# Optimization experiments

Hardware: AMD Instinct MI355X
Metric: run time of the kernel (lower is better)

Reference implementation:

```python
import jax, jax.numpy as jnp
import numpy as np
import math

BATCH, L, H, P = 8, 2048, 1024, 512
DT_MIN, DT_MAX = 1e-3, 1e-1
STEP_RESCALE = 1.0


def setup_inputs() -> dict:
    key = jax.random.key(0)
    ks = jax.random.split(key, 8)
    signal = jax.random.normal(ks[0], (BATCH, L, H), dtype=jnp.float32)
    prev_state = jnp.zeros((BATCH, P), dtype=jnp.float32)
    # S5-style init: Lambda_re < 0, Lambda_im = pi * k
    Lambda_re = -0.5 * jnp.ones((P,), dtype=jnp.float32)
    Lambda_im = math.pi * jnp.arange(P, dtype=jnp.float32)
    # B stored as real (P,H,2) -> complex B_tilde; lecun scale 1/sqrt(H)
    B = jax.random.normal(ks[1], (P, H, 2), dtype=jnp.float32) / math.sqrt(H)
    # C stored as real (H,P,2) -> complex C_tilde; lecun scale 1/sqrt(P)
    C = jax.random.normal(ks[2], (H, P, 2), dtype=jnp.float32) / math.sqrt(P)
    D = jax.random.normal(ks[3], (H,), dtype=jnp.float32)
    u = jax.random.uniform(ks[4], (P, 1), dtype=jnp.float32)
    log_step = u * (math.log(DT_MAX) - math.log(DT_MIN)) + math.log(DT_MIN)
    return {"signal": signal, "prev_state": prev_state,
            "Lambda_re": Lambda_re, "Lambda_im": Lambda_im,
            "B": B, "C": C, "D": D, "log_step": log_step}


def _binop(qi, qj):
    # parallel-scan combine for diagonal linear recurrence x_t = A_t x_{t-1} + b_t
    A_i, b_i = qi
    A_j, b_j = qj
    return (A_j * A_i, b_j + A_j * b_i)


def reference(signal, prev_state, Lambda_re, Lambda_im, B, C, D, log_step):
    Lambda = Lambda_re + 1j * Lambda_im                      # (P,) complex
    B_tilde = B[..., 0] + 1j * B[..., 1]                     # (P,H)
    C_tilde = C[..., 0] + 1j * C[..., 1]                     # (H,P)
    step = STEP_RESCALE * jnp.exp(log_step[:, 0])            # (P,)
    # zero-order hold discretization
    Lambda_bar = jnp.exp(Lambda * step)                      # (P,)
    B_bar = ((Lambda_bar - 1.0) / Lambda)[:, None] * B_tilde # (P,H)
    # Bu elements: (BATCH, L, P) complex
    Bu = jnp.einsum('blh,ph->blp', signal.astype(B_bar.dtype), B_bar)
    # A elements: Lambda_bar tiled over time; first element carries prev_state
    A_first = (Lambda_bar[None, :] * prev_state.astype(Lambda_bar.dtype))[:, None, :]
    A_rest = jnp.broadcast_to(Lambda_bar, (signal.shape[0], signal.shape[1] - 1, Lambda_bar.shape[0]))
    A = jnp.concatenate([A_first, A_rest], axis=1)           # (BATCH, L, P)
    _, xs = jax.lax.associative_scan(_binop, (A, Bu), axis=1)  # xs: (BATCH, L, P)
    # conj_sym=True -> 2 * Re(C_tilde @ x), plus feedthrough D*u
    y = 2.0 * jnp.einsum('blp,hp->blh', xs, C_tilde).real + D * signal
    state = xs[:, -1]                                        # (BATCH, P) complex
    return y, state
```

## Files before the change

### kernel.cpp

```cpp
#include <hip/hip_runtime.h>
#include <math.h>

#define L_SEQ   2048
#define BATCH_N 8
#define H_DIM   1024
#define P_DIM   512
#define M_DIM   (BATCH_N * L_SEQ)
#define N2      1024
#define NC      16
#define T_CHUNK 128

typedef __attribute__((ext_vector_type(8))) __bf16 bf16x8;
typedef __attribute__((ext_vector_type(4))) float f32x4;

__device__ __forceinline__ unsigned f2bf_bits(float f) {
    unsigned u = __builtin_bit_cast(unsigned, f);
    return (u + 0x7fffu + ((u >> 16) & 1u)) >> 16;
}
__device__ __forceinline__ float bf_lo(unsigned v) {
    return __builtin_bit_cast(float, v << 16);
}
__device__ __forceinline__ float bf_hi(unsigned v) {
    return __builtin_bit_cast(float, v & 0xffff0000u);
}
__device__ __forceinline__ float bf2f(unsigned short u) {
    return __builtin_bit_cast(float, (unsigned)u << 16);
}

#define ASYNC_COPY16(gsrc, ldst)                                            \
    __builtin_amdgcn_global_load_lds(                                       \
        (__attribute__((address_space(1))) void*)(gsrc),                    \
        (__attribute__((address_space(3))) void*)(ldst), 16, 0, 0)

__global__ void setup_lam(const float* __restrict__ Lre_in,
                          const float* __restrict__ Lim_in,
                          const float* __restrict__ log_step,
                          float* __restrict__ lam) {
    int p = blockIdx.x * blockDim.x + threadIdx.x;
    if (p >= P_DIM) return;
    float step = expf(log_step[p]);
    float c = Lre_in[p];
    float d = Lim_in[p];
    float mag = expf(c * step);
    float ang = d * step;
    float lr = mag * cosf(ang);
    float li = mag * sinf(ang);
    float a = lr - 1.0f, b = li;
    float inv = 1.0f / (c * c + d * d);
    lam[p]             = lr;
    lam[P_DIM + p]     = li;
    lam[2 * P_DIM + p] = (a * c + b * d) * inv;
    lam[3 * P_DIM + p] = (b * c - a * d) * inv;
}

__global__ void build_W(const float* __restrict__ B,
                        const float* __restrict__ C,
                        const float* __restrict__ lam,
                        unsigned short* __restrict__ W1,
                        unsigned short* __restrict__ W2) {
    int idx = blockIdx.x * blockDim.x + threadIdx.x;
    if (idx < P_DIM * H_DIM) {
        int p = idx >> 10;
        int h = idx & (H_DIM - 1);
        float bre = B[(size_t)idx * 2];
        float bim = B[(size_t)idx * 2 + 1];
        float gre = lam[2 * P_DIM + p];
        float gim = lam[3 * P_DIM + p];
        W1[(size_t)p * H_DIM + h]           = (unsigned short)f2bf_bits(gre * bre - gim * bim);
        W1[(size_t)(P_DIM + p) * H_DIM + h] = (unsigned short)f2bf_bits(gre * bim + gim * bre);
    } else {
        int j = idx - P_DIM * H_DIM;
        int h = j >> 9;
        int p = j & (P_DIM - 1);
        float cre = C[(size_t)j * 2];
        float cim = C[(size_t)j * 2 + 1];
        W2[(size_t)h * N2 + p]         = (unsigned short)f2bf_bits( 2.0f * cre);
        W2[(size_t)h * N2 + P_DIM + p] = (unsigned short)f2bf_bits(-2.0f * cim);
    }
}

__global__ void convert_sig(const float* __restrict__ in,
                            unsigned short* __restrict__ out) {
    size_t i = ((size_t)blockIdx.x * 256 + threadIdx.x) * 4;
    float4 v = *(const float4*)(in + i);
    ushort4 o;
    o.x = (unsigned short)f2bf_bits(v.x);
    o.y = (unsigned short)f2bf_bits(v.y);
    o.z = (unsigned short)f2bf_bits(v.z);
    o.w = (unsigned short)f2bf_bits(v.w);
    *(ushort4*)(out + i) = o;
}

template <int MODE>
__global__ __launch_bounds__(256) void gemm_mfma(
    const unsigned short* __restrict__ A,
    const unsigned short* __restrict__ W,
    void* __restrict__ Out, int K,
    const float* __restrict__ Dvec, const unsigned short* __restrict__ SigBf)
{
    __shared__ unsigned short smem[128 * 32 * 2];
    unsigned short* As = smem;
    unsigned short* Ws = smem + 128 * 32;

    const int tid  = threadIdx.x;
    const int lane = tid & 63;
    const int wid  = tid >> 6;
    const int wm   = wid >> 1;
    const int wn   = wid & 1;

    const int id  = blockIdx.x;
    const int xcd = id & 7;
    const int j   = id >> 3;
    const int mb  = xcd * 16 + (j >> 3);
    const int nb  = j & 7;
    const int m0 = mb * 128;
    const int n0 = nb * 128;

    const int r0 = tid >> 2;
    const int kq = (tid & 3) * 8;
    const unsigned short* Ag0 = A + (size_t)(m0 + r0) * K + kq;
    const unsigned short* Ag1 = Ag0 + (size_t)64 * K;
    const unsigned short* Wg0 = W + (size_t)(n0 + r0) * K + kq;
    const unsigned short* Wg1 = Wg0 + (size_t)64 * K;
    unsigned short* Ad0 = As + (size_t)(wid * 64) * 8;
    unsigned short* Ad1 = As + (size_t)(256 + wid * 64) * 8;
    unsigned short* Wd0 = Ws + (size_t)(wid * 64) * 8;
    unsigned short* Wd1 = Ws + (size_t)(256 + wid * 64) * 8;

    const int fr = lane & 15;
    const int fq = lane >> 4;

    f32x4 acc[4][4] = {};

    for (int k0 = 0; k0 < K; k0 += 32) {
        __syncthreads();
        ASYNC_COPY16(Ag0 + k0, Ad0);
        ASYNC_COPY16(Ag1 + k0, Ad1);
        ASYNC_COPY16(Wg0 + k0, Wd0);
        ASYNC_COPY16(Wg1 + k0, Wd1);
        __syncthreads();

        bf16x8 af[4], wf[4];
        #pragma unroll
        for (int mi = 0; mi < 4; ++mi)
            af[mi] = *(const bf16x8*)&As[(size_t)(wm * 64 + mi * 16 + fr) * 32 + fq * 8];
        #pragma unroll
        for (int ni = 0; ni < 4; ++ni)
            wf[ni] = *(const bf16x8*)&Ws[(size_t)(wn * 64 + ni * 16 + fr) * 32 + fq * 8];
        #pragma unroll
        for (int mi = 0; mi < 4; ++mi)
            #pragma unroll
            for (int ni = 0; ni < 4; ++ni)
                acc[mi][ni] = __builtin_amdgcn_mfma_f32_16x16x32_bf16(
                    af[mi], wf[ni], acc[mi][ni], 0, 0, 0);
    }

    if (MODE == 0) {
        unsigned short* T = smem;
        #pragma unroll
        for (int h = 0; h < 2; ++h) {
            __syncthreads();
            if (wm == h) {
                #pragma unroll
                for (int mi = 0; mi < 4; ++mi)
                    #pragma unroll
                    for (int ni = 0; ni < 4; ++ni)
                        #pragma unroll
                        for (int r = 0; r < 4; ++r) {
                            int lrow = mi * 16 + fq * 4 + r;
                            int lcol = wn * 64 + ni * 16 + fr;
                            T[lrow * 128 + lcol] =
                                (unsigned short)f2bf_bits(acc[mi][ni][r]);
                        }
            }
            __syncthreads();
            #pragma unroll
            for (int jj = 0; jj < 4; ++jj) {
                int chunk = jj * 256 + tid;
                int row = chunk >> 4;
                int co  = (chunk & 15) * 8;
                *(ulonglong2*)((unsigned short*)Out +
                    (size_t)(m0 + h * 64 + row) * 1024 + n0 + co) =
                    *(const ulonglong2*)&T[row * 128 + co];
            }
        }
    } else {
        #pragma unroll
        for (int mi = 0; mi < 4; ++mi) {
            #pragma unroll
            for (int ni = 0; ni < 4; ++ni) {
                #pragma unroll
                for (int r = 0; r < 4; ++r) {
                    int row = m0 + wm * 64 + mi * 16 + fq * 4 + r;
                    int col = n0 + wn * 64 + ni * 16 + fr;
                    float v = acc[mi][ni][r];
                    v = fmaf(Dvec[col], bf2f(SigBf[(size_t)row * 1024 + col]), v);
                    ((float*)Out)[(size_t)row * 1024 + col] = v;
                }
            }
        }
    }
}

__global__ __launch_bounds__(256) void scan_sums(
    const unsigned short* __restrict__ Bu, const float* __restrict__ lam,
    float* __restrict__ S)
{
    int b = blockIdx.x, c = blockIdx.y, t = threadIdx.x;
    int p0 = 2 * t, p1 = 2 * t + 1;
    float lr0 = lam[p0], li0 = lam[P_DIM + p0];
    float lr1 = lam[p1], li1 = lam[P_DIM + p1];
    const unsigned* base =
        (const unsigned*)(Bu + ((size_t)b * L_SEQ + (size_t)c * T_CHUNK) * N2);
    float xr0 = 0, xi0 = 0, xr1 = 0, xi1 = 0;
    for (int j0 = 0; j0 < T_CHUNK; j0 += 8) {
        unsigned R[8], I[8];
        #pragma unroll
        for (int j = 0; j < 8; ++j) {
            R[j] = base[(size_t)(j0 + j) * 512 + t];
            I[j] = base[(size_t)(j0 + j) * 512 + 256 + t];
        }
        #pragma unroll
        for (int j = 0; j < 8; ++j) {
            float nr0 = fmaf(lr0, xr0, fmaf(-li0, xi0, bf_lo(R[j])));
            float ni0 = fmaf(lr0, xi0, fmaf( li0, xr0, bf_lo(I[j])));
            float nr1 = fmaf(lr1, xr1, fmaf(-li1, xi1, bf_hi(R[j])));
            float ni1 = fmaf(lr1, xi1, fmaf( li1, xr1, bf_hi(I[j])));
            xr0 = nr0; xi0 = ni0; xr1 = nr1; xi1 = ni1;
        }
    }
    float* Sb = S + ((size_t)(b * NC + c) * 2) * P_DIM;
    Sb[p0] = xr0; Sb[p1] = xr1;
    Sb[P_DIM + p0] = xi0; Sb[P_DIM + p1] = xi1;
}

__global__ __launch_bounds__(512) void scan_carry(
    const float* __restrict__ S, const float* __restrict__ lam,
    float* __restrict__ CIN)
{
    int b = blockIdx.x, p = threadIdx.x;
    float lr = lam[p], li = lam[P_DIM + p];
    float pr = lr, pi = li;
    #pragma unroll
    for (int i = 0; i < 7; ++i) {
        float nr = pr * pr - pi * pi;
        float ni = 2.0f * pr * pi;
        pr = nr; pi = ni;
    }
    float cr = 0, ci = 0;
    for (int c = 0; c < NC; ++c) {
        float* Cb = CIN + ((size_t)(b * NC + c) * 2) * P_DIM;
        Cb[p] = cr; Cb[P_DIM + p] = ci;
        const float* Sb = S + ((size_t)(b * NC + c) * 2) * P_DIM;
        float sr = Sb[p], si = Sb[P_DIM + p];
        float nr = fmaf(pr, cr, fmaf(-pi, ci, sr));
        float ni = fmaf(pr, ci, fmaf( pi, cr, si));
        cr = nr; ci = ni;
    }
}

__global__ __launch_bounds__(256) void scan_apply(
    unsigned short* __restrict__ Bu, const float* __restrict__ lam,
    const float* __restrict__ CIN, float* __restrict__ out_state,
    int interleaved)
{
    int b = blockIdx.x, c = blockIdx.y, t = threadIdx.x;
    int p0 = 2 * t, p1 = 2 * t + 1;
    float lr0 = lam[p0], li0 = lam[P_DIM + p0];
    float lr1 = lam[p1], li1 = lam[P_DIM + p1];
    const float* Cb = CIN + ((size_t)(b * NC + c) * 2) * P_DIM;
    float xr0 = Cb[p0], xi0 = Cb[P_DIM + p0];
    float xr1 = Cb[p1], xi1 = Cb[P_DIM + p1];
    unsigned* base =
        (unsigned*)(Bu + ((size_t)b * L_SEQ + (size_t)c * T_CHUNK) * N2);
    for (int j0 = 0; j0 < T_CHUNK; j0 += 8) {
        unsigned R[8], I[8];
        #pragma unroll
        for (int j = 0; j < 8; ++j) {
            R[j] = base[(size_t)(j0 + j) * 512 + t];
            I[j] = base[(size_t)(j0 + j) * 512 + 256 + t];
        }
        #pragma unroll
        for (int j = 0; j < 8; ++j) {
            float nr0 = fmaf(lr0, xr0, fmaf(-li0, xi0, bf_lo(R[j])));
            float ni0 = fmaf(lr0, xi0, fmaf( li0, xr0, bf_lo(I[j])));
            float nr1 = fmaf(lr1, xr1, fmaf(-li1, xi1, bf_hi(R[j])));
            float ni1 = fmaf(lr1, xi1, fmaf( li1, xr1, bf_hi(I[j])));
            xr0 = nr0; xi0 = ni0; xr1 = nr1; xi1 = ni1;
            R[j] = f2bf_bits(nr0) | (f2bf_bits(nr1) << 16);
            I[j] = f2bf_bits(ni0) | (f2bf_bits(ni1) << 16);
        }
        #pragma unroll
        for (int j = 0; j < 8; ++j) {
            base[(size_t)(j0 + j) * 512 + t]       = R[j];
            base[(size_t)(j0 + j) * 512 + 256 + t] = I[j];
        }
    }
    if (c == NC - 1) {
        if (interleaved) {
            out_state[((size_t)b * P_DIM + p0) * 2]     = xr0;
            out_state[((size_t)b * P_DIM + p0) * 2 + 1] = xi0;
            out_state[((size_t)b * P_DIM + p1) * 2]     = xr1;
            out_state[((size_t)b * P_DIM + p1) * 2 + 1] = xi1;
        } else {
            out_state[(size_t)b * P_DIM + p0] = xr0;
            out_state[(size_t)b * P_DIM + p1] = xr1;
        }
    }
}

extern "C" void kernel_launch(void* const* d_in, const int* in_sizes, int n_in,
                              void* d_out, int out_size, void* d_ws, size_t ws_size,
                              hipStream_t stream)
{
    const float* signal   = (const float*)d_in[0];
    const float* Lre      = (const float*)d_in[2];
    const float* Lim      = (const float*)d_in[3];
    const float* B        = (const float*)d_in[4];
    const float* C        = (const float*)d_in[5];
    const float* Dv       = (const float*)d_in[6];
    const float* log_step = (const float*)d_in[7];

    char* ws = (char*)d_ws;
    unsigned short* sigbf = (unsigned short*)ws;
    unsigned short* Bubf  = (unsigned short*)(ws + 33554432);
    unsigned short* W1bf  = (unsigned short*)(ws + 67108864);
    unsigned short* W2bf  = (unsigned short*)(ws + 69206016);
    float*          lam   = (float*)(ws + 71303168);
    float*          S     = (float*)(ws + 71311360);
    float*          CIN   = (float*)(ws + 71835648);
    size_t need = 72359936;
    if (ws_size < need) return;

    float* y_out = (float*)d_out;
    float* state_out = y_out + (size_t)M_DIM * H_DIM;
    int interleaved = (out_size - M_DIM * H_DIM) >= 2 * BATCH_N * P_DIM;

    setup_lam<<<dim3(2), dim3(256), 0, stream>>>(Lre, Lim, log_step, lam);
    build_W<<<dim3((2 * P_DIM * H_DIM) / 256), dim3(256), 0, stream>>>(
        B, C, lam, W1bf, W2bf);
    convert_sig<<<dim3((M_DIM * H_DIM) / 1024), dim3(256), 0, stream>>>(signal, sigbf);

    gemm_mfma<0><<<dim3(1024), dim3(256), 0, stream>>>(
        sigbf, W1bf, Bubf, H_DIM, nullptr, nullptr);

    scan_sums<<<dim3(BATCH_N, NC), dim3(256), 0, stream>>>(Bubf, lam, S);
    scan_carry<<<dim3(BATCH_N), dim3(512), 0, stream>>>(S, lam, CIN);
    scan_apply<<<dim3(BATCH_N, NC), dim3(256), 0, stream>>>(
        Bubf, lam, CIN, state_out, interleaved);

    gemm_mfma<1><<<dim3(1024), dim3(256), 0, stream>>>(
        Bubf, W2bf, y_out, N2, Dv, sigbf);
}
```

Baseline: 273.0 us.

## Enlarge GEMM tiles to 256x128 with K=64 swizzled LDS and halve scan chunks

The MFMA GEMM now uses 256x128 output tiles with a K-step of 64. Each wave computes 64x128 using an XOR-style swizzled LDS layout to avoid bank conflicts, and the grid is halved to 512 blocks. The epilogue hoists the D vector loads. The scan is split into 32 chunks of 64 steps instead of 16 of 128, with the carry power loop adjusted to match, to expose more scan parallelism. The larger accumulator array raises register pressure and LDS use and still runs without double-buffering.

Measured after the change: 234.2 us. 1.17x faster.

```diff
diff --git a/kernel.cpp b/kernel.cpp
--- a/kernel.cpp
+++ b/kernel.cpp
@@ -7,8 +7,8 @@
 #define P_DIM   512
 #define M_DIM   (BATCH_N * L_SEQ)
 #define N2      1024
-#define NC      16
-#define T_CHUNK 128
+#define NC      32
+#define T_CHUNK 64
 
 typedef __attribute__((ext_vector_type(8))) __bf16 bf16x8;
 typedef __attribute__((ext_vector_type(4))) float f32x4;
@@ -92,67 +92,74 @@
 }
 
 template <int MODE>
-__global__ __launch_bounds__(256) void gemm_mfma(
+__global__ __launch_bounds__(256, 2) void gemm_mfma(
     const unsigned short* __restrict__ A,
     const unsigned short* __restrict__ W,
     void* __restrict__ Out, int K,
     const float* __restrict__ Dvec, const unsigned short* __restrict__ SigBf)
 {
-    __shared__ unsigned short smem[128 * 32 * 2];
+    __shared__ unsigned short smem[256 * 64 + 128 * 64];
     unsigned short* As = smem;
-    unsigned short* Ws = smem + 128 * 32;
+    unsigned short* Ws = smem + 256 * 64;
 
     const int tid  = threadIdx.x;
     const int lane = tid & 63;
     const int wid  = tid >> 6;
-    const int wm   = wid >> 1;
-    const int wn   = wid & 1;
+    const int wm   = wid;
 
     const int id  = blockIdx.x;
     const int xcd = id & 7;
     const int j   = id >> 3;
-    const int mb  = xcd * 16 + (j >> 3);
+    const int mb  = xcd * 8 + (j >> 3);
     const int nb  = j & 7;
-    const int m0 = mb * 128;
+    const int m0 = mb * 256;
     const int n0 = nb * 128;
 
-    const int r0 = tid >> 2;
-    const int kq = (tid & 3) * 8;
-    const unsigned short* Ag0 = A + (size_t)(m0 + r0) * K + kq;
-    const unsigned short* Ag1 = Ag0 + (size_t)64 * K;
-    const unsigned short* Wg0 = W + (size_t)(n0 + r0) * K + kq;
-    const unsigned short* Wg1 = Wg0 + (size_t)64 * K;
-    unsigned short* Ad0 = As + (size_t)(wid * 64) * 8;
-    unsigned short* Ad1 = As + (size_t)(256 + wid * 64) * 8;
-    unsigned short* Wd0 = Ws + (size_t)(wid * 64) * 8;
-    unsigned short* Wd1 = Ws + (size_t)(256 + wid * 64) * 8;
+    const int srow = tid >> 3;
+    const int qg   = ((tid & 7) - ((tid >> 4) & 7)) & 7;
+    const unsigned short* Abase = A + (size_t)(m0 + srow) * K + qg * 8;
+    const unsigned short* Wbase = W + (size_t)(n0 + srow) * K + qg * 8;
 
     const int fr = lane & 15;
-    const int fq = lane >> 4;
-
-    f32x4 acc[4][4] = {};
-
-    for (int k0 = 0; k0 < K; k0 += 32) {
+    const int fq = (lane >> 4) & 3;
+    const int sw = fr >> 1;
+
+    f32x4 acc[4][8] = {};
+
+    for (int k0 = 0; k0 < K; k0 += 64) {
         __syncthreads();
-        ASYNC_COPY16(Ag0 + k0, Ad0);
-        ASYNC_COPY16(Ag1 + k0, Ad1);
-        ASYNC_COPY16(Wg0 + k0, Wd0);
-        ASYNC_COPY16(Wg1 + k0, Wd1);
+        #pragma unroll
+        for (int i = 0; i < 8; ++i)
+            ASYNC_COPY16(Abase + (size_t)(i * 32) * K + k0,
+                         As + (size_t)(i * 256 + wid * 64) * 8);
+        #pragma unroll
+        for (int i = 0; i < 4; ++i)
+            ASYNC_COPY16(Wbase + (size_t)(i * 32) * K + k0,
+                         Ws + (size_t)(i * 256 + wid * 64) * 8);
         __syncthreads();
 
-        bf16x8 af[4], wf[4];
-        #pragma unroll
-        for (int mi = 0; mi < 4; ++mi)
-            af[mi] = *(const bf16x8*)&As[(size_t)(wm * 64 + mi * 16 + fr) * 32 + fq * 8];
-        #pragma unroll
-        for (int ni = 0; ni < 4; ++ni)
-            wf[ni] = *(const bf16x8*)&Ws[(size_t)(wn * 64 + ni * 16 + fr) * 32 + fq * 8];
-        #pragma unroll
-        for (int mi = 0; mi < 4; ++mi)
-            #pragma unroll
-            for (int ni = 0; ni < 4; ++ni)
-                acc[mi][ni] = __builtin_amdgcn_mfma_f32_16x16x32_bf16(
-                    af[mi], wf[ni], acc[mi][ni], 0, 0, 0);
+        #pragma unroll
+        for (int kk = 0; kk < 2; ++kk) {
+            bf16x8 af[4], wf[8];
+            #pragma unroll
+            for (int mi = 0; mi < 4; ++mi) {
+                int row = wm * 64 + mi * 16 + fr;
+                int sl  = (kk * 4 + fq + sw) & 7;
+                af[mi] = *(const bf16x8*)&As[(size_t)row * 64 + sl * 8];
+            }
+            #pragma unroll
+            for (int ni = 0; ni < 8; ++ni) {
+                int row = ni * 16 + fr;
+                int sl  = (kk * 4 + fq + sw) & 7;
+                wf[ni] = *(const bf16x8*)&Ws[(size_t)row * 64 + sl * 8];
+            }
+            #pragma unroll
+            for (int mi = 0; mi < 4; ++mi)
+                #pragma unroll
+                for (int ni = 0; ni < 8; ++ni)
+                    acc[mi][ni] = __builtin_amdgcn_mfma_f32_16x16x32_bf16(
+                        af[mi], wf[ni], acc[mi][ni], 0, 0, 0);
+        }
     }
 
     if (MODE == 0) {
@@ -160,41 +167,46 @@
         #pragma unroll
         for (int h = 0; h < 2; ++h) {
             __syncthreads();
-            if (wm == h) {
+            if ((wm >> 1) == h) {
+                unsigned short* Tw = T + (wm & 1) * 8192;
                 #pragma unroll
                 for (int mi = 0; mi < 4; ++mi)
                     #pragma unroll
-                    for (int ni = 0; ni < 4; ++ni)
+                    for (int ni = 0; ni < 8; ++ni)
                         #pragma unroll
                         for (int r = 0; r < 4; ++r) {
                             int lrow = mi * 16 + fq * 4 + r;
-                            int lcol = wn * 64 + ni * 16 + fr;
-                            T[lrow * 128 + lcol] =
+                            int lcol = ni * 16 + fr;
+                            Tw[lrow * 128 + lcol] =
                                 (unsigned short)f2bf_bits(acc[mi][ni][r]);
                         }
             }
             __syncthreads();
             #pragma unroll
-            for (int jj = 0; jj < 4; ++jj) {
+            for (int jj = 0; jj < 8; ++jj) {
                 int chunk = jj * 256 + tid;
-                int row = chunk >> 4;
-                int co  = (chunk & 15) * 8;
+                int grow  = chunk >> 4;
+                int co    = (chunk & 15) * 8;
                 *(ulonglong2*)((unsigned short*)Out +
-                    (size_t)(m0 + h * 64 + row) * 1024 + n0 + co) =
-                    *(const ulonglong2*)&T[row * 128 + co];
+                    (size_t)(m0 + h * 128 + grow) * 1024 + n0 + co) =
+                    *(const ulonglong2*)&T[grow * 128 + co];
             }
         }
     } else {
+        float Dl[8];
+        #pragma unroll
+        for (int ni = 0; ni < 8; ++ni)
+            Dl[ni] = Dvec[n0 + ni * 16 + fr];
         #pragma unroll
         for (int mi = 0; mi < 4; ++mi) {
             #pragma unroll
-            for (int ni = 0; ni < 4; ++ni) {
+            for (int ni = 0; ni < 8; ++ni) {
                 #pragma unroll
                 for (int r = 0; r < 4; ++r) {
                     int row = m0 + wm * 64 + mi * 16 + fq * 4 + r;
-                    int col = n0 + wn * 64 + ni * 16 + fr;
+                    int col = n0 + ni * 16 + fr;
                     float v = acc[mi][ni][r];
-                    v = fmaf(Dvec[col], bf2f(SigBf[(size_t)row * 1024 + col]), v);
+                    v = fmaf(Dl[ni], bf2f(SigBf[(size_t)row * 1024 + col]), v);
                     ((float*)Out)[(size_t)row * 1024 + col] = v;
                 }
             }
@@ -242,7 +254,7 @@
     float lr = lam[p], li = lam[P_DIM + p];
     float pr = lr, pi = li;
     #pragma unroll
-    for (int i = 0; i < 7; ++i) {
+    for (int i = 0; i < 6; ++i) {
         float nr = pr * pr - pi * pi;
         float ni = 2.0f * pr * pi;
         pr = nr; pi = ni;
@@ -341,7 +353,7 @@
         B, C, lam, W1bf, W2bf);
     convert_sig<<<dim3((M_DIM * H_DIM) / 1024), dim3(256), 0, stream>>>(signal, sigbf);
 
-    gemm_mfma<0><<<dim3(1024), dim3(256), 0, stream>>>(
+    gemm_mfma<0><<<dim3(512), dim3(256), 0, stream>>>(
         sigbf, W1bf, Bubf, H_DIM, nullptr, nullptr);
 
     scan_sums<<<dim3(BATCH_N, NC), dim3(256), 0, stream>>>(Bubf, lam, S);
@@ -349,6 +361,6 @@
     scan_apply<<<dim3(BATCH_N, NC), dim3(256), 0, stream>>>(
         Bubf, lam, CIN, state_out, interleaved);
 
-    gemm_mfma<1><<<dim3(1024), dim3(256), 0, stream>>>(
+    gemm_mfma<1><<<dim3(512), dim3(256), 0, stream>>>(
         Bubf, W2bf, y_out, N2, Dv, sigbf);
 }
```
